# Kernel tuning notes

Hardware: AMD Instinct MI355X
Metric: run time of the kernel (lower is better)

## Reference

```python
import jax, jax.numpy as jnp
import numpy as np
from collections import deque


def _build_graph_paths(N, E, seed=0):
    """Random directed graph; all-pairs BFS shortest paths (matches nx.shortest_path on
    the unweighted DiGraph). Returns flattened (pair_id, node_id) membership lists:
    for every reachable pair (i,j) and every node e on the shortest path i->j, one
    entry with pair_id=i*N+j, node_id=e. path_len[i*N+j] = number of nodes on the
    path (0 if unreachable)."""
    rng = np.random.default_rng(seed)
    src = rng.integers(0, N, E)
    dst = rng.integers(0, N, E)
    adj = [[] for _ in range(N)]
    for u, v in zip(src, dst):
        adj[u].append(int(v))
    pair_chunks, node_chunks = [], []
    path_len = np.zeros(N * N, dtype=np.int32)
    for s in range(N):
        dist = np.full(N, -1, np.int32)
        parent = np.full(N, -1, np.int32)
        dist[s] = 0
        parent[s] = s
        q = deque([s])
        while q:
            u = q.popleft()
            for v in adj[u]:
                if dist[v] < 0:
                    dist[v] = dist[u] + 1
                    parent[v] = u
                    q.append(v)
        reach = np.nonzero(dist >= 0)[0].astype(np.int32)
        path_len[s * N + reach] = dist[reach] + 1
        cur = reach.copy()
        rem = dist[reach].copy()          # steps remaining (records rem+1 nodes)
        pid = (s * N + reach).astype(np.int64)
        while cur.size:
            pair_chunks.append(pid.copy())
            node_chunks.append(cur.copy())
            m = rem > 0                   # keep walking toward the source
            cur = parent[cur[m]]
            rem = rem[m] - 1
            pid = pid[m]
    pair_id = np.concatenate(pair_chunks).astype(np.int32)
    node_id = np.concatenate(node_chunks).astype(np.int32)
    return pair_id, node_id, path_len


def setup_inputs() -> dict:
    N, DIM, H, E = 1024, 64, 16, 8192
    pair_id, node_id, path_len = _build_graph_paths(N, E, seed=0)
    key = jax.random.key(0)
    k1, k2, k3, k4 = jax.random.split(key, 4)
    x = jax.random.normal(k1, (N, DIM), jnp.float32)
    edge_attr = jax.random.normal(k2, (N, 4), jnp.float32)
    lim = 1.0 / np.sqrt(4.0)              # nn.Linear(4, H) default init range
    W = jax.random.uniform(k3, (H, 4), jnp.float32, -lim, lim)
    b = jax.random.uniform(k4, (H,), jnp.float32, -lim, lim)
    return {
        "x": x,
        "edge_attr": edge_attr,
        "W": W,
        "b": b,
        "pair_id": jnp.asarray(pair_id),
        "node_id": jnp.asarray(node_id),
        "path_len": jnp.asarray(path_len),
    }


def reference(x, edge_attr, W, b, pair_id, node_id, path_len):
    # Original: out[i,j] = mean_{e in shortest_path(i,j)} (W @ edge_attr[e] + b),
    # 0 where no path. Implemented as gather + segment_sum + one small GEMM
    # (exactly equal by linearity of the Linear layer).
    N = x.shape[0]
    H = W.shape[0]
    gathered = edge_attr[node_id]                                   # [P, 4]
    sums = jax.ops.segment_sum(gathered, pair_id, num_segments=N * N)  # [N*N, 4]
    L = path_len[:, None].astype(sums.dtype)                        # [N*N, 1]
    lin = sums @ W.T + L * b                                        # sum of per-node Linear outputs
    out = jnp.where(path_len[:, None] > 0, lin / jnp.maximum(L, 1.0), 0.0)
    out = out.reshape(N, N, H)
    return jnp.transpose(out, (2, 0, 1))                            # 'h w n -> n h w'
```

## Files before the change

### kernel.cpp

```cpp
#include <hip/hip_runtime.h>


#define BS 256
#define NW 4
#define KPT 4
#define NMAX 1024

typedef float f32x4 __attribute__((ext_vector_type(4)));
typedef int   i32x4 __attribute__((ext_vector_type(4)));

__global__ __launch_bounds__(BS, 8) void ee_fused(
    const float* __restrict__ edge_attr,
    const float* __restrict__ W,
    const float* __restrict__ b,
    const int*   __restrict__ pair_id,
    const int*   __restrict__ node_id,
    const int*   __restrict__ path_len,
    float*       __restrict__ out,
    int N, int NN, int P)
{
    __shared__ __align__(16) f32x4 psum[NMAX];
    __shared__ float sW[64];
    __shared__ float sbv[16];
    __shared__ int wcnt1[NW];
    __shared__ int wcnt0[NW];
    __shared__ int smaxw[NW];
    __shared__ int slo;

    const int tid   = threadIdx.x;
    const int wave  = tid >> 6;
    const int lane  = tid & 63;
    const int s     = blockIdx.x;
    const int sbase = s * N;

    if (tid == 0) slo = 0;
    if (tid < 64) sW[tid]  = W[tid];
    if (tid < 16) sbv[tid] = b[tid];

    const i32x4 Lv = *reinterpret_cast<const i32x4*>(path_len + sbase + 4 * tid);
    int L[KPT] = { Lv.x, Lv.y, Lv.z, Lv.w };

    unsigned long long b1[KPT];
    int wtot1 = 0, wtot0 = 0, m = 0;
#pragma unroll
    for (int c = 0; c < KPT; ++c) {
        b1[c] = __ballot(L[c] > 1);
        const unsigned long long b0 = __ballot(L[c] > 0);
        wtot1 += __popcll(b1[c]);
        wtot0 += __popcll(b0);
        m = max(m, L[c]);
    }
    for (int o = 32; o > 0; o >>= 1) m = max(m, __shfl_down(m, o));
    if (lane == 0) { wcnt1[wave] = wtot1; wcnt0[wave] = wtot0; smaxw[wave] = m; }

    if (wave == 0 && P > 0) {
        int lo = 0, hi = P;
        while (hi > lo) {
            const int span = hi - lo;
            const int p = lo + (int)(((long long)span * lane) >> 6);
            const int v = pair_id[p];
            const unsigned long long bal = __ballot(v >= sbase);
            if (bal == 0ull) {
                lo += (int)(((long long)span * 63) >> 6) + 1;
            } else {
                const int f = (int)__builtin_ctzll(bal);
                if (f == 0) {
                    hi = lo;
                } else {
                    const int pf   = lo + (int)(((long long)span * f) >> 6);
                    const int pfm1 = lo + (int)(((long long)span * (f - 1)) >> 6);
                    lo = pfm1 + 1;
                    hi = pf;
                }
            }
        }
        if (lane == 0) slo = lo;
    }
    __syncthreads();
    const int lo = slo;

    int n0 = 0, maxd = 0, prew = 0;
#pragma unroll
    for (int w = 0; w < NW; ++w) {
        n0  += wcnt0[w];
        maxd = max(maxd, smaxw[w]);
        if (w < wave) prew += wcnt1[w];
    }
    const unsigned long long below = (1ull << lane) - 1ull;
    int prelane = prew;
#pragma unroll
    for (int c = 0; c < KPT; ++c) prelane += __popcll(b1[c] & below);

    int par[KPT];
    {
        int prec = 0;
#pragma unroll
        for (int c = 0; c < KPT; ++c) {
            par[c] = 0;
            if (L[c] > 1)
                par[c] = node_id[lo + n0 + prelane + prec];
            prec += (L[c] > 1);
        }
    }

    f32x4 acc[KPT];
#pragma unroll
    for (int c = 0; c < KPT; ++c) acc[c] = (f32x4)0.f;

    for (int d = 0; d < maxd; ++d) {
#pragma unroll
        for (int c = 0; c < KPT; ++c) {
            if (L[c] == d + 1) {
                const int j = 4 * tid + c;
                f32x4 e = *reinterpret_cast<const f32x4*>(edge_attr + 4 * j);
                if (d) e += psum[par[c]];
                acc[c] = e;
                psum[j] = e;
            }
        }
        __syncthreads();
    }

    float fmul[KPT], gmul[KPT];
#pragma unroll
    for (int c = 0; c < KPT; ++c) {
        fmul[c] = (L[c] > 0) ? 1.0f / (float)L[c] : 0.0f;
        gmul[c] = (L[c] > 0) ? 1.0f : 0.0f;
    }
#pragma unroll
    for (int h = 0; h < 16; ++h) {
        const float w0 = sW[4 * h + 0], w1 = sW[4 * h + 1];
        const float w2 = sW[4 * h + 2], w3 = sW[4 * h + 3];
        const float bh = sbv[h];
        f32x4 v;
#pragma unroll
        for (int c = 0; c < KPT; ++c)
            v[c] = (acc[c].x * w0 + acc[c].y * w1 +
                    acc[c].z * w2 + acc[c].w * w3) * fmul[c] + bh * gmul[c];
        reinterpret_cast<f32x4*>(out + (size_t)h * NN + sbase)[tid] = v;
    }
}

extern "C" void kernel_launch(void* const* d_in, const int* in_sizes, int n_in,
                              void* d_out, int out_size, void* d_ws, size_t ws_size,
                              hipStream_t stream) {
    const float* edge_attr = (const float*)d_in[1];
    const float* W         = (const float*)d_in[2];
    const float* b         = (const float*)d_in[3];
    const int*   pair_id   = (const int*)d_in[4];
    const int*   node_id   = (const int*)d_in[5];
    const int*   path_len  = (const int*)d_in[6];
    const int P  = in_sizes[4];
    const int NN = in_sizes[6];
    const int N  = in_sizes[0] / 64;

    ee_fused<<<N, BS, 0, stream>>>(edge_attr, W, b, pair_id, node_id, path_len,
                                   (float*)d_out, N, NN, P);
}
```

Measured before the change: 114.4 us.

## Process four sources per block with 512 threads and shared edge_attr loads

```diff
diff --git a/kernel.cpp b/kernel.cpp
--- a/kernel.cpp
+++ b/kernel.cpp
@@ -1,15 +1,17 @@
 #include <hip/hip_runtime.h>
 
 
-#define BS 256
-#define NW 4
-#define KPT 4
+#define BS 512
+#define NW 8
+#define KPT 2
+#define SPB 4
 #define NMAX 1024
 
 typedef float f32x4 __attribute__((ext_vector_type(4)));
-typedef int   i32x4 __attribute__((ext_vector_type(4)));
+typedef float f32x2 __attribute__((ext_vector_type(2)));
+typedef int   i32x2 __attribute__((ext_vector_type(2)));
 
-__global__ __launch_bounds__(BS, 8) void ee_fused(
+__global__ __launch_bounds__(BS, 2) void ee_fused(
     const float* __restrict__ edge_attr,
     const float* __restrict__ W,
     const float* __restrict__ b,
@@ -22,44 +24,63 @@
     __shared__ __align__(16) f32x4 psum[NMAX];
     __shared__ float sW[64];
     __shared__ float sbv[16];
-    __shared__ int wcnt1[NW];
-    __shared__ int wcnt0[NW];
-    __shared__ int smaxw[NW];
-    __shared__ int slo;
+    __shared__ int wcnt1[SPB][NW];
+    __shared__ int wcnt0[SPB][NW];
+    __shared__ int wmax [SPB][NW];
+    __shared__ int slo[SPB];
 
-    const int tid   = threadIdx.x;
-    const int wave  = tid >> 6;
-    const int lane  = tid & 63;
-    const int s     = blockIdx.x;
-    const int sbase = s * N;
+    const int tid  = threadIdx.x;
+    const int wave = tid >> 6;
+    const int lane = tid & 63;
+    const int s0   = blockIdx.x * SPB;
 
-    if (tid == 0) slo = 0;
-    if (tid < 64) sW[tid]  = W[tid];
-    if (tid < 16) sbv[tid] = b[tid];
+    if (tid < SPB) slo[tid] = 0;
+    if (tid < 64)  sW[tid]  = W[tid];
+    if (tid < 16)  sbv[tid] = b[tid];
 
-    const i32x4 Lv = *reinterpret_cast<const i32x4*>(path_len + sbase + 4 * tid);
-    int L[KPT] = { Lv.x, Lv.y, Lv.z, Lv.w };
+    const int j0 = 2 * tid, j1 = 2 * tid + 1;
 
-    unsigned long long b1[KPT];
-    int wtot1 = 0, wtot0 = 0, m = 0;
+    f32x4 ea0 = (f32x4)0.f, ea1 = (f32x4)0.f;
+    if (j0 < N) ea0 = *reinterpret_cast<const f32x4*>(edge_attr + 4 * j0);
+    if (j1 < N) ea1 = *reinterpret_cast<const f32x4*>(edge_attr + 4 * j1);
+
+    int L[SPB][KPT];
+    unsigned long long b1[SPB][KPT];
 #pragma unroll
-    for (int c = 0; c < KPT; ++c) {
-        b1[c] = __ballot(L[c] > 1);
-        const unsigned long long b0 = __ballot(L[c] > 0);
-        wtot1 += __popcll(b1[c]);
-        wtot0 += __popcll(b0);
-        m = max(m, L[c]);
+    for (int t = 0; t < SPB; ++t) {
+        const int s = s0 + t;
+        int l0 = 0, l1 = 0;
+        if (s < N) {
+            if (j1 < N) {
+                const i32x2 lv =
+                    *reinterpret_cast<const i32x2*>(path_len + (size_t)s * N + j0);
+                l0 = lv.x; l1 = lv.y;
+            } else if (j0 < N) {
+                l0 = path_len[(size_t)s * N + j0];
+            }
+        }
+        L[t][0] = l0; L[t][1] = l1;
+        b1[t][0] = __ballot(l0 > 1);
+        b1[t][1] = __ballot(l1 > 1);
+        const int c0 = __popcll(__ballot(l0 > 0)) + __popcll(__ballot(l1 > 0));
+        int m = max(l0, l1);
+        for (int o = 32; o > 0; o >>= 1) m = max(m, __shfl_down(m, o));
+        if (lane == 0) {
+            wcnt1[t][wave] = __popcll(b1[t][0]) + __popcll(b1[t][1]);
+            wcnt0[t][wave] = c0;
+            wmax [t][wave] = m;
+        }
     }
-    for (int o = 32; o > 0; o >>= 1) m = max(m, __shfl_down(m, o));
-    if (lane == 0) { wcnt1[wave] = wtot1; wcnt0[wave] = wtot0; smaxw[wave] = m; }
+    __syncthreads();
 
-    if (wave == 0 && P > 0) {
+    if (wave < SPB && P > 0 && (s0 + wave) < N) {
+        const int target = (s0 + wave) * N;
         int lo = 0, hi = P;
         while (hi > lo) {
             const int span = hi - lo;
             const int p = lo + (int)(((long long)span * lane) >> 6);
             const int v = pair_id[p];
-            const unsigned long long bal = __ballot(v >= sbase);
+            const unsigned long long bal = __ballot(v >= target);
             if (bal == 0ull) {
                 lo += (int)(((long long)span * 63) >> 6) + 1;
             } else {
@@ -74,70 +95,69 @@
                 }
             }
         }
-        if (lane == 0) slo = lo;
+        if (lane == 0) slo[wave] = lo;
     }
     __syncthreads();
-    const int lo = slo;
 
-    int n0 = 0, maxd = 0, prew = 0;
+    const unsigned long long below = (1ull << lane) - 1ull;
+    int par[SPB][KPT];
+    int maxdv[SPB];
 #pragma unroll
-    for (int w = 0; w < NW; ++w) {
-        n0  += wcnt0[w];
-        maxd = max(maxd, smaxw[w]);
-        if (w < wave) prew += wcnt1[w];
-    }
-    const unsigned long long below = (1ull << lane) - 1ull;
-    int prelane = prew;
+    for (int t = 0; t < SPB; ++t) {
+        int n0 = 0, maxd = 0, prew = 0;
 #pragma unroll
-    for (int c = 0; c < KPT; ++c) prelane += __popcll(b1[c] & below);
-
-    int par[KPT];
-    {
-        int prec = 0;
-#pragma unroll
-        for (int c = 0; c < KPT; ++c) {
-            par[c] = 0;
-            if (L[c] > 1)
-                par[c] = node_id[lo + n0 + prelane + prec];
-            prec += (L[c] > 1);
+        for (int w = 0; w < NW; ++w) {
+            n0  += wcnt0[t][w];
+            maxd = max(maxd, wmax[t][w]);
+            if (w < wave) prew += wcnt1[t][w];
         }
+        maxdv[t] = maxd;
+        const int prelane = prew + __popcll(b1[t][0] & below)
+                                 + __popcll(b1[t][1] & below);
+        const int base = slo[t] + n0 + prelane;
+        par[t][0] = 0; par[t][1] = 0;
+        if (L[t][0] > 1) par[t][0] = node_id[base];
+        if (L[t][1] > 1) par[t][1] = node_id[base + (L[t][0] > 1 ? 1 : 0)];
     }
 
-    f32x4 acc[KPT];
+    for (int t = 0; t < SPB; ++t) {
+        const int s = s0 + t;
+        if (s >= N) break;
+        f32x4 acc0 = (f32x4)0.f, acc1 = (f32x4)0.f;
+        const int maxd = maxdv[t];
+        for (int d = 0; d < maxd; ++d) {
+            if (L[t][0] == d + 1) {
+                f32x4 e = ea0;
+                if (d) e += psum[par[t][0]];
+                acc0 = e; psum[j0] = e;
+            }
+            if (L[t][1] == d + 1) {
+                f32x4 e = ea1;
+                if (d) e += psum[par[t][1]];
+                acc1 = e; psum[j1] = e;
+            }
+            asm volatile("s_waitcnt lgkmcnt(0)" ::: "memory");
+            __builtin_amdgcn_s_barrier();
+        }
+        const float f0 = (L[t][0] > 0) ? 1.0f / (float)L[t][0] : 0.0f;
+        const float g0 = (L[t][0] > 0) ? 1.0f : 0.0f;
+        const float f1 = (L[t][1] > 0) ? 1.0f / (float)L[t][1] : 0.0f;
+        const float g1 = (L[t][1] > 0) ? 1.0f : 0.0f;
 #pragma unroll
-    for (int c = 0; c < KPT; ++c) acc[c] = (f32x4)0.f;
-
-    for (int d = 0; d < maxd; ++d) {
-#pragma unroll
-        for (int c = 0; c < KPT; ++c) {
-            if (L[c] == d + 1) {
-                const int j = 4 * tid + c;
-                f32x4 e = *reinterpret_cast<const f32x4*>(edge_attr + 4 * j);
-                if (d) e += psum[par[c]];
-                acc[c] = e;
-                psum[j] = e;
+        for (int h = 0; h < 16; ++h) {
+            const float w0 = sW[4 * h + 0], w1 = sW[4 * h + 1];
+            const float w2 = sW[4 * h + 2], w3 = sW[4 * h + 3];
+            const float bh = sbv[h];
+            f32x2 v;
+            v.x = (acc0.x * w0 + acc0.y * w1 + acc0.z * w2 + acc0.w * w3) * f0 + bh * g0;
+            v.y = (acc1.x * w0 + acc1.y * w1 + acc1.z * w2 + acc1.w * w3) * f1 + bh * g1;
+            float* o = out + (size_t)h * NN + (size_t)s * N;
+            if (j1 < N) {
+                reinterpret_cast<f32x2*>(o)[tid] = v;
+            } else if (j0 < N) {
+                o[j0] = v.x;
             }
         }
-        __syncthreads();
-    }
-
-    float fmul[KPT], gmul[KPT];
-#pragma unroll
-    for (int c = 0; c < KPT; ++c) {
-        fmul[c] = (L[c] > 0) ? 1.0f / (float)L[c] : 0.0f;
-        gmul[c] = (L[c] > 0) ? 1.0f : 0.0f;
-    }
-#pragma unroll
-    for (int h = 0; h < 16; ++h) {
-        const float w0 = sW[4 * h + 0], w1 = sW[4 * h + 1];
-        const float w2 = sW[4 * h + 2], w3 = sW[4 * h + 3];
-        const float bh = sbv[h];
-        f32x4 v;
-#pragma unroll
-        for (int c = 0; c < KPT; ++c)
-            v[c] = (acc[c].x * w0 + acc[c].y * w1 +
-                    acc[c].z * w2 + acc[c].w * w3) * fmul[c] + bh * gmul[c];
-        reinterpret_cast<f32x4*>(out + (size_t)h * NN + sbase)[tid] = v;
     }
 }
 
@@ -154,6 +174,7 @@
     const int NN = in_sizes[6];
     const int N  = in_sizes[0] / 64;
 
-    ee_fused<<<N, BS, 0, stream>>>(edge_attr, W, b, pair_id, node_id, path_len,
-                                   (float*)d_out, N, NN, P);
+    const int grid = (N + SPB - 1) / SPB;
+    ee_fused<<<grid, BS, 0, stream>>>(edge_attr, W, b, pair_id, node_id, path_len,
+                                      (float*)d_out, N, NN, P);
 }
```

Result: slower. 118.5 us (+3.6%).

## Replace binary search for row offset with prefix sum of path lengths

Applied to the files above, without the earlier changes.

```diff
diff --git a/kernel.cpp b/kernel.cpp
--- a/kernel.cpp
+++ b/kernel.cpp
@@ -9,15 +9,32 @@
 typedef float f32x4 __attribute__((ext_vector_type(4)));
 typedef int   i32x4 __attribute__((ext_vector_type(4)));
 
-__global__ __launch_bounds__(BS, 8) void ee_fused(
+__global__ __launch_bounds__(BS) void ee_rowsum(
+    const int* __restrict__ path_len, int* __restrict__ rowsum, int N)
+{
+    __shared__ int wred[NW];
+    const int tid  = threadIdx.x;
+    const int wave = tid >> 6;
+    const int lane = tid & 63;
+    const int s    = blockIdx.x;
+    const i32x4 lv =
+        *reinterpret_cast<const i32x4*>(path_len + (size_t)s * N + 4 * tid);
+    int v = lv.x + lv.y + lv.z + lv.w;
+    for (int o = 32; o > 0; o >>= 1) v += __shfl_down(v, o);
+    if (lane == 0) wred[wave] = v;
+    __syncthreads();
+    if (tid == 0) rowsum[s] = wred[0] + wred[1] + wred[2] + wred[3];
+}
+
+__global__ __launch_bounds__(BS, 4) void ee_fused(
     const float* __restrict__ edge_attr,
     const float* __restrict__ W,
     const float* __restrict__ b,
-    const int*   __restrict__ pair_id,
     const int*   __restrict__ node_id,
     const int*   __restrict__ path_len,
+    const int*   __restrict__ rowsum,
     float*       __restrict__ out,
-    int N, int NN, int P)
+    int N, int NN)
 {
     __shared__ __align__(16) f32x4 psum[NMAX];
     __shared__ float sW[64];
@@ -25,7 +42,7 @@
     __shared__ int wcnt1[NW];
     __shared__ int wcnt0[NW];
     __shared__ int smaxw[NW];
-    __shared__ int slo;
+    __shared__ int wlo[NW];
 
     const int tid   = threadIdx.x;
     const int wave  = tid >> 6;
@@ -33,12 +50,26 @@
     const int s     = blockIdx.x;
     const int sbase = s * N;
 
-    if (tid == 0) slo = 0;
     if (tid < 64) sW[tid]  = W[tid];
     if (tid < 16) sbv[tid] = b[tid];
 
+    f32x4 ea[KPT];
+#pragma unroll
+    for (int c = 0; c < KPT; ++c)
+        ea[c] = *reinterpret_cast<const f32x4*>(edge_attr + 4 * (4 * tid + c));
+
     const i32x4 Lv = *reinterpret_cast<const i32x4*>(path_len + sbase + 4 * tid);
     int L[KPT] = { Lv.x, Lv.y, Lv.z, Lv.w };
+
+    {
+        const i32x4 rv = *reinterpret_cast<const i32x4*>(rowsum + 4 * tid);
+        int part = 0;
+#pragma unroll
+        for (int c = 0; c < KPT; ++c)
+            if (4 * tid + c < s) part += rv[c];
+        for (int o = 32; o > 0; o >>= 1) part += __shfl_down(part, o);
+        if (lane == 0) wlo[wave] = part;
+    }
 
     unsigned long long b1[KPT];
     int wtot1 = 0, wtot0 = 0, m = 0;
@@ -52,38 +83,14 @@
     }
     for (int o = 32; o > 0; o >>= 1) m = max(m, __shfl_down(m, o));
     if (lane == 0) { wcnt1[wave] = wtot1; wcnt0[wave] = wtot0; smaxw[wave] = m; }
+    __syncthreads();
 
-    if (wave == 0 && P > 0) {
-        int lo = 0, hi = P;
-        while (hi > lo) {
-            const int span = hi - lo;
-            const int p = lo + (int)(((long long)span * lane) >> 6);
-            const int v = pair_id[p];
-            const unsigned long long bal = __ballot(v >= sbase);
-            if (bal == 0ull) {
-                lo += (int)(((long long)span * 63) >> 6) + 1;
-            } else {
-                const int f = (int)__builtin_ctzll(bal);
-                if (f == 0) {
-                    hi = lo;
-                } else {
-                    const int pf   = lo + (int)(((long long)span * f) >> 6);
-                    const int pfm1 = lo + (int)(((long long)span * (f - 1)) >> 6);
-                    lo = pfm1 + 1;
-                    hi = pf;
-                }
-            }
-        }
-        if (lane == 0) slo = lo;
-    }
-    __syncthreads();
-    const int lo = slo;
-
-    int n0 = 0, maxd = 0, prew = 0;
+    int n0 = 0, maxd = 0, prew = 0, lo = 0;
 #pragma unroll
     for (int w = 0; w < NW; ++w) {
         n0  += wcnt0[w];
         maxd = max(maxd, smaxw[w]);
+        lo  += wlo[w];
         if (w < wave) prew += wcnt1[w];
     }
     const unsigned long long below = (1ull << lane) - 1ull;
@@ -111,11 +118,10 @@
 #pragma unroll
         for (int c = 0; c < KPT; ++c) {
             if (L[c] == d + 1) {
-                const int j = 4 * tid + c;
-                f32x4 e = *reinterpret_cast<const f32x4*>(edge_attr + 4 * j);
+                f32x4 e = ea[c];
                 if (d) e += psum[par[c]];
                 acc[c] = e;
-                psum[j] = e;
+                psum[4 * tid + c] = e;
             }
         }
         __syncthreads();
@@ -147,13 +153,14 @@
     const float* edge_attr = (const float*)d_in[1];
     const float* W         = (const float*)d_in[2];
     const float* b         = (const float*)d_in[3];
-    const int*   pair_id   = (const int*)d_in[4];
     const int*   node_id   = (const int*)d_in[5];
     const int*   path_len  = (const int*)d_in[6];
-    const int P  = in_sizes[4];
     const int NN = in_sizes[6];
     const int N  = in_sizes[0] / 64;
 
-    ee_fused<<<N, BS, 0, stream>>>(edge_attr, W, b, pair_id, node_id, path_len,
-                                   (float*)d_out, N, NN, P);
+    int* rowsum = (int*)d_ws;
+
+    ee_rowsum<<<N, BS, 0, stream>>>(path_len, rowsum, N);
+    ee_fused<<<N, BS, 0, stream>>>(edge_attr, W, b, node_id, path_len, rowsum,
+                                   (float*)d_out, N, NN);
 }
```

Result: no change. 113.2 us (-1.0%).
